# Performance work log

Measured on AMD Instinct MI355X. Metric: run time of the kernel, lower is better.

## Reference

```python
import jax, jax.numpy as jnp
import numpy as np

HARD_ANGLE = 15.0  # degrees, from PMLoss __init__ default
NUM_CLASSES = 22
NUM_POINTS = 2048
BATCH = 32


def quat_to_rotmat(q):
    # q: [..., 4] in (w, x, y, z) order (PoseCNN convention); assumes unit norm
    w, x, y, z = q[..., 0], q[..., 1], q[..., 2], q[..., 3]
    R = jnp.stack([
        1 - 2 * (y * y + z * z), 2 * (x * y - z * w), 2 * (x * z + y * w),
        2 * (x * y + z * w), 1 - 2 * (x * x + z * z), 2 * (y * z - x * w),
        2 * (x * z - y * w), 2 * (y * z + x * w), 1 - 2 * (x * x + y * y)],
        axis=-1)
    return R.reshape(q.shape[:-1] + (3, 3))


def smooth_l1(x):
    ax = jnp.abs(x)
    return jnp.where(ax < 1.0, 0.5 * x * x, ax - 0.5)


def setup_inputs() -> dict:
    key = jax.random.key(0)
    k1, k2, k3, k4 = jax.random.split(key, 4)
    B, C, P = BATCH, NUM_CLASSES, NUM_POINTS
    # unit quaternions per (sample, class)
    q_pred = jax.random.normal(k1, (B, C, 4), dtype=jnp.float32)
    q_pred = q_pred / jnp.linalg.norm(q_pred, axis=-1, keepdims=True)
    q_gt = jax.random.normal(k2, (B, C, 4), dtype=jnp.float32)
    q_gt = q_gt / jnp.linalg.norm(q_gt, axis=-1, keepdims=True)
    prediction = q_pred.reshape(B, 4 * C)
    target = q_gt.reshape(B, 4 * C)
    # one active class per sample: weight block of ones at that class
    cls = jax.random.randint(k3, (B,), 1, C)  # skip background class 0
    weight = jnp.zeros((B, C, 4), dtype=jnp.float32)
    weight = weight.at[jnp.arange(B), cls, :].set(1.0).reshape(B, 4 * C)
    # model point clouds, roughly object-scale (~10 cm)
    points = 0.1 * jax.random.normal(k4, (C, P, 3), dtype=jnp.float32)
    # half the classes symmetric
    symmetry = (jnp.arange(C) % 2).astype(jnp.float32)
    return {"prediction": prediction, "target": target, "weight": weight,
            "points": points, "symmetry": symmetry}


def reference(prediction, target, weight, points, symmetry):
    B = prediction.shape[0]
    C = symmetry.shape[0]
    P = points.shape[1]
    # class per sample = first class with weight > 0 (CUDA scans stride-4 w slot)
    wsel = weight.reshape(B, C, 4)[:, :, 0]           # [B, C]
    cls = jnp.argmax(wsel > 0, axis=1)                # [B]
    valid = (jnp.max(wsel, axis=1) > 0)               # [B] samples with a class
    bidx = jnp.arange(B)
    q_pred = prediction.reshape(B, C, 4)[bidx, cls]   # [B, 4]
    q_gt = target.reshape(B, C, 4)[bidx, cls]         # [B, 4]
    R_pred = quat_to_rotmat(q_pred)                   # [B, 3, 3]
    R_gt = quat_to_rotmat(q_gt)
    pts = points[cls]                                 # [B, P, 3]
    p_pred = jnp.einsum('bij,bpj->bpi', R_pred, pts)  # [B, P, 3]
    p_gt = jnp.einsum('bij,bpj->bpi', R_gt, pts)      # [B, P, 3]
    # angular distance between quaternions, in degrees
    dot = jnp.abs(jnp.sum(q_pred * q_gt, axis=1))
    ang = 2.0 * jnp.arccos(jnp.clip(dot, 0.0, 1.0)) * (180.0 / jnp.pi)
    use_closest = (symmetry[cls] > 0) & (ang > HARD_ANGLE)  # [B]
    # pairwise squared distances without materializing [B,P,P,3]
    d2 = (jnp.sum(p_pred * p_pred, axis=-1)[:, :, None]
          + jnp.sum(p_gt * p_gt, axis=-1)[:, None, :]
          - 2.0 * jnp.einsum('bpi,bqi->bpq', p_pred, p_gt))  # [B, P, P]
    nn_idx = jnp.argmin(d2, axis=-1)                         # [B, P]
    p_gt_nn = jnp.take_along_axis(p_gt, nn_idx[..., None], axis=1)
    matched = jnp.where(use_closest[:, None, None], p_gt_nn, p_gt)
    diff = p_pred - matched                                   # [B, P, 3]
    per_sample = jnp.sum(smooth_l1(diff), axis=(1, 2)) * valid.astype(diff.dtype)
    loss = jnp.sum(per_sample) / jnp.asarray(B * P, dtype=diff.dtype)
    return loss
```

## Files before the change

### kernel.cpp

```cpp
#include <hip/hip_runtime.h>

#define NPTS 2048
#define QC 32
#define G  (NPTS / QC)
#define RP 8
#define HARD_COS 0.9914448613738104f
#define META_FLOATS 8
#define PRED_OFF 1024


__global__ __launch_bounds__(256) void pm_setup(const float* __restrict__ pred,
                                                const float* __restrict__ tgt,
                                                const float* __restrict__ wgt,
                                                const float* __restrict__ sym,
                                                const float* __restrict__ points,
                                                float* __restrict__ ws,
                                                float* __restrict__ out,
                                                int B, int C, int gt_off) {
    const int b = blockIdx.y;
    const int side = blockIdx.x;

    int cls = 0; float valid = 0.0f;
    for (int c = 0; c < C; ++c) {
        if (wgt[b * 4 * C + c * 4] > 0.0f) { cls = c; valid = 1.0f; break; }
    }

    const float* q = (side == 0 ? pred : tgt) + b * 4 * C + cls * 4;
    const float w = q[0], x = q[1], y = q[2], z = q[3];
    const float m0 = 1.f - 2.f * (y * y + z * z);
    const float m1 = 2.f * (x * y - z * w);
    const float m2 = 2.f * (x * z + y * w);
    const float m3 = 2.f * (x * y + z * w);
    const float m4 = 1.f - 2.f * (x * x + z * z);
    const float m5 = 2.f * (y * z - x * w);
    const float m6 = 2.f * (x * z - y * w);
    const float m7 = 2.f * (y * z + x * w);
    const float m8 = 1.f - 2.f * (x * x + y * y);

    const float* pts = points + (size_t)cls * NPTS * 3;
    float4* dst = (float4*)(ws + (side == 0 ? PRED_OFF : gt_off)) + (size_t)b * NPTS;
    const int tid = threadIdx.x;
    if (valid != 0.0f) {
#pragma unroll
        for (int r = 0; r < RP; ++r) {
            int i = r * 256 + tid;
            float px = pts[i * 3 + 0], py = pts[i * 3 + 1], pz = pts[i * 3 + 2];
            float ax = m0 * px + m1 * py + m2 * pz;
            float ay = m3 * px + m4 * py + m5 * pz;
            float az = m6 * px + m7 * py + m8 * pz;
            float ww = (side == 0) ? 0.0f : (ax * ax + ay * ay + az * az);
            dst[i] = make_float4(ax, ay, az, ww);
        }
    }

    if (side == 0 && tid == 0) {
        const float* qp = pred + b * 4 * C + cls * 4;
        const float* qg = tgt  + b * 4 * C + cls * 4;
        float dot = fabsf(qp[0] * qg[0] + qp[1] * qg[1] + qp[2] * qg[2] + qp[3] * qg[3]);
        dot = fminf(fmaxf(dot, 0.0f), 1.0f);
        float uc = (sym[cls] > 0.0f && dot < HARD_COS) ? 1.0f : 0.0f;
        ws[b * META_FLOATS + 0] = valid;
        ws[b * META_FLOATS + 1] = uc;
        if (b == 0) out[0] = 0.0f;
    }
}

__global__ __launch_bounds__(256) void pm_partial(float* __restrict__ ws,
                                                  int gt_off, int cand_off) {
    const int b  = blockIdx.y;
    const int qc = blockIdx.x;
    if (ws[b * META_FLOATS + 0] == 0.0f || ws[b * META_FLOATS + 1] == 0.0f) return;

    const float4* pred_rot = (const float4*)(ws + PRED_OFF) + (size_t)b * NPTS;
    const float4* gt_rot   = (const float4*)(ws + gt_off)   + (size_t)b * NPTS;
    const int tid = threadIdx.x;

    __shared__ float4 gt[G];
    if (tid < G) gt[tid] = gt_rot[qc * G + tid];
    __syncthreads();

    float nx[RP], ny[RP], nz[RP], bd[RP];
    int bi[RP];
#pragma unroll
    for (int r = 0; r < RP; ++r) {
        float4 pp = pred_rot[r * 256 + tid];
        nx[r] = -2.0f * pp.x; ny[r] = -2.0f * pp.y; nz[r] = -2.0f * pp.z;
        bd[r] = 3.4e38f; bi[r] = 0;
    }

#pragma unroll 4
    for (int j = 0; j < G; ++j) {
        float4 g = gt[j];
#pragma unroll
        for (int r = 0; r < RP; ++r) {
            float d = __fmaf_rn(nx[r], g.x,
                      __fmaf_rn(ny[r], g.y,
                      __fmaf_rn(nz[r], g.z, g.w)));
            if (d < bd[r]) { bd[r] = d; bi[r] = j; }
        }
    }

    float2* cand = (float2*)(ws + cand_off) + ((size_t)b * QC + qc) * NPTS;
#pragma unroll
    for (int r = 0; r < RP; ++r) {
        int p = r * 256 + tid;
        cand[p] = make_float2(bd[r], (float)(qc * G + bi[r]));
    }
}

__device__ __forceinline__ float smooth_l1(float x) {
    float ax = fabsf(x);
    return (ax < 1.0f) ? 0.5f * x * x : ax - 0.5f;
}

__global__ __launch_bounds__(256) void pm_final(float* __restrict__ ws,
                                                float* __restrict__ out,
                                                int gt_off, int cand_off,
                                                float inv_bp) {
    __shared__ float partial[4];
    const int b = blockIdx.y;
    const int tid = threadIdx.x;
    float acc = 0.0f;

    if (ws[b * META_FLOATS + 0] != 0.0f) {
        const float4* pred_rot = (const float4*)(ws + PRED_OFF) + (size_t)b * NPTS;
        const float4* gt_rot   = (const float4*)(ws + gt_off)   + (size_t)b * NPTS;
        const int p = blockIdx.x * 256 + tid;
        float4 pp = pred_rot[p];
        float4 g;
        if (ws[b * META_FLOATS + 1] != 0.0f) {
            const float2* cand = (const float2*)(ws + cand_off) + (size_t)b * QC * NPTS + p;
            float bd = 3.4e38f; int bq = 0;
#pragma unroll
            for (int qc = 0; qc < QC; ++qc) {
                float2 cq = cand[(size_t)qc * NPTS];
                if (cq.x < bd) { bd = cq.x; bq = (int)cq.y; }
            }
            g = gt_rot[bq];
        } else {
            g = gt_rot[p];
        }
        acc = smooth_l1(pp.x - g.x) + smooth_l1(pp.y - g.y) + smooth_l1(pp.z - g.z);
    }

    for (int off = 32; off > 0; off >>= 1) acc += __shfl_down(acc, off);
    if ((tid & 63) == 0) partial[tid >> 6] = acc;
    __syncthreads();
    if (tid == 0) {
        float s = partial[0] + partial[1] + partial[2] + partial[3];
        atomicAdd(out, s * inv_bp);
    }
}

extern "C" void kernel_launch(void* const* d_in, const int* in_sizes, int n_in,
                              void* d_out, int out_size, void* d_ws, size_t ws_size,
                              hipStream_t stream) {
    const float* pred = (const float*)d_in[0];
    const float* tgt  = (const float*)d_in[1];
    const float* wgt  = (const float*)d_in[2];
    const float* pts  = (const float*)d_in[3];
    const float* sym  = (const float*)d_in[4];
    float* out = (float*)d_out;
    float* ws  = (float*)d_ws;

    const int C = in_sizes[4];
    const int B = in_sizes[0] / (4 * C);

    const int gt_off   = PRED_OFF + B * NPTS * 4;
    const int cand_off = gt_off   + B * NPTS * 4;

    dim3 gridS(2, B);
    pm_setup<<<gridS, 256, 0, stream>>>(pred, tgt, wgt, sym, pts, ws, out, B, C, gt_off);
    dim3 gridP(QC, B);
    pm_partial<<<gridP, 256, 0, stream>>>(ws, gt_off, cand_off);
    dim3 gridF(NPTS / 256, B);
    pm_final<<<gridF, 256, 0, stream>>>(ws, out, gt_off, cand_off,
                                        1.0f / (float)(B * NPTS));
}
```

Baseline: 107.1 us.

## Fuse setup kernel into scan and final by recomputing rotated points on the fly

Removes the separate setup kernel that wrote rotated pred/gt point clouds to workspace. The scan and final kernels now derive the class and use-closest flag themselves, build the rotation matrices, and rotate points directly from the model point cloud. This saves one kernel launch and the workspace round-trip, at the cost of redundant meta scans and rotations in every block.

Result: faster. 104.8 us (-2.1%).

```diff
diff --git a/kernel.cpp b/kernel.cpp
--- a/kernel.cpp
+++ b/kernel.cpp
@@ -5,88 +5,89 @@
 #define G  (NPTS / QC)
 #define RP 8
 #define HARD_COS 0.9914448613738104f
-#define META_FLOATS 8
-#define PRED_OFF 1024
 
 
-__global__ __launch_bounds__(256) void pm_setup(const float* __restrict__ pred,
-                                                const float* __restrict__ tgt,
-                                                const float* __restrict__ wgt,
-                                                const float* __restrict__ sym,
-                                                const float* __restrict__ points,
-                                                float* __restrict__ ws,
-                                                float* __restrict__ out,
-                                                int B, int C, int gt_off) {
-    const int b = blockIdx.y;
-    const int side = blockIdx.x;
+struct Meta { int cls; bool valid; bool uc; };
 
-    int cls = 0; float valid = 0.0f;
+__device__ __forceinline__ Meta get_meta(const float* __restrict__ pred,
+                                         const float* __restrict__ tgt,
+                                         const float* __restrict__ wgt,
+                                         const float* __restrict__ sym,
+                                         int b, int C) {
+    Meta m; m.cls = 0; m.valid = false;
     for (int c = 0; c < C; ++c) {
-        if (wgt[b * 4 * C + c * 4] > 0.0f) { cls = c; valid = 1.0f; break; }
+        if (wgt[b * 4 * C + c * 4] > 0.0f) { m.cls = c; m.valid = true; break; }
     }
-
-    const float* q = (side == 0 ? pred : tgt) + b * 4 * C + cls * 4;
-    const float w = q[0], x = q[1], y = q[2], z = q[3];
-    const float m0 = 1.f - 2.f * (y * y + z * z);
-    const float m1 = 2.f * (x * y - z * w);
-    const float m2 = 2.f * (x * z + y * w);
-    const float m3 = 2.f * (x * y + z * w);
-    const float m4 = 1.f - 2.f * (x * x + z * z);
-    const float m5 = 2.f * (y * z - x * w);
-    const float m6 = 2.f * (x * z - y * w);
-    const float m7 = 2.f * (y * z + x * w);
-    const float m8 = 1.f - 2.f * (x * x + y * y);
-
-    const float* pts = points + (size_t)cls * NPTS * 3;
-    float4* dst = (float4*)(ws + (side == 0 ? PRED_OFF : gt_off)) + (size_t)b * NPTS;
-    const int tid = threadIdx.x;
-    if (valid != 0.0f) {
-#pragma unroll
-        for (int r = 0; r < RP; ++r) {
-            int i = r * 256 + tid;
-            float px = pts[i * 3 + 0], py = pts[i * 3 + 1], pz = pts[i * 3 + 2];
-            float ax = m0 * px + m1 * py + m2 * pz;
-            float ay = m3 * px + m4 * py + m5 * pz;
-            float az = m6 * px + m7 * py + m8 * pz;
-            float ww = (side == 0) ? 0.0f : (ax * ax + ay * ay + az * az);
-            dst[i] = make_float4(ax, ay, az, ww);
-        }
-    }
-
-    if (side == 0 && tid == 0) {
-        const float* qp = pred + b * 4 * C + cls * 4;
-        const float* qg = tgt  + b * 4 * C + cls * 4;
-        float dot = fabsf(qp[0] * qg[0] + qp[1] * qg[1] + qp[2] * qg[2] + qp[3] * qg[3]);
-        dot = fminf(fmaxf(dot, 0.0f), 1.0f);
-        float uc = (sym[cls] > 0.0f && dot < HARD_COS) ? 1.0f : 0.0f;
-        ws[b * META_FLOATS + 0] = valid;
-        ws[b * META_FLOATS + 1] = uc;
-        if (b == 0) out[0] = 0.0f;
-    }
+    const float* qp = pred + b * 4 * C + m.cls * 4;
+    const float* qg = tgt  + b * 4 * C + m.cls * 4;
+    float dot = fabsf(qp[0] * qg[0] + qp[1] * qg[1] + qp[2] * qg[2] + qp[3] * qg[3]);
+    dot = fminf(fmaxf(dot, 0.0f), 1.0f);
+    m.uc = m.valid && (sym[m.cls] > 0.0f) && (dot < HARD_COS);
+    return m;
 }
 
-__global__ __launch_bounds__(256) void pm_partial(float* __restrict__ ws,
-                                                  int gt_off, int cand_off) {
+__device__ __forceinline__ void quat_rotmat(const float* __restrict__ q, float* m) {
+    float w = q[0], x = q[1], y = q[2], z = q[3];
+    m[0] = 1.f - 2.f * (y * y + z * z);
+    m[1] = 2.f * (x * y - z * w);
+    m[2] = 2.f * (x * z + y * w);
+    m[3] = 2.f * (x * y + z * w);
+    m[4] = 1.f - 2.f * (x * x + z * z);
+    m[5] = 2.f * (y * z - x * w);
+    m[6] = 2.f * (x * z - y * w);
+    m[7] = 2.f * (y * z + x * w);
+    m[8] = 1.f - 2.f * (x * x + y * y);
+}
+
+__device__ __forceinline__ float smooth_l1(float x) {
+    float ax = fabsf(x);
+    return (ax < 1.0f) ? 0.5f * x * x : ax - 0.5f;
+}
+
+__global__ __launch_bounds__(256) void pm_scan(const float* __restrict__ pred,
+                                               const float* __restrict__ tgt,
+                                               const float* __restrict__ wgt,
+                                               const float* __restrict__ sym,
+                                               const float* __restrict__ points,
+                                               float* __restrict__ ws,
+                                               float* __restrict__ out, int C) {
     const int b  = blockIdx.y;
     const int qc = blockIdx.x;
-    if (ws[b * META_FLOATS + 0] == 0.0f || ws[b * META_FLOATS + 1] == 0.0f) return;
-
-    const float4* pred_rot = (const float4*)(ws + PRED_OFF) + (size_t)b * NPTS;
-    const float4* gt_rot   = (const float4*)(ws + gt_off)   + (size_t)b * NPTS;
     const int tid = threadIdx.x;
 
+    if (b == 0 && qc == 0 && tid == 0) out[0] = 0.0f;
+
+    Meta mt = get_meta(pred, tgt, wgt, sym, b, C);
+    if (!mt.valid || !mt.uc) return;
+
+    float Rp[9], Rg[9];
+    quat_rotmat(pred + b * 4 * C + mt.cls * 4, Rp);
+    quat_rotmat(tgt  + b * 4 * C + mt.cls * 4, Rg);
+    const float* pts = points + (size_t)mt.cls * NPTS * 3;
+
     __shared__ float4 gt[G];
-    if (tid < G) gt[tid] = gt_rot[qc * G + tid];
-    __syncthreads();
+    if (tid < G) {
+        int i = qc * G + tid;
+        float x = pts[i * 3 + 0], y = pts[i * 3 + 1], z = pts[i * 3 + 2];
+        float ax = Rg[0] * x + Rg[1] * y + Rg[2] * z;
+        float ay = Rg[3] * x + Rg[4] * y + Rg[5] * z;
+        float az = Rg[6] * x + Rg[7] * y + Rg[8] * z;
+        gt[tid] = make_float4(ax, ay, az, ax * ax + ay * ay + az * az);
+    }
 
     float nx[RP], ny[RP], nz[RP], bd[RP];
     int bi[RP];
 #pragma unroll
     for (int r = 0; r < RP; ++r) {
-        float4 pp = pred_rot[r * 256 + tid];
-        nx[r] = -2.0f * pp.x; ny[r] = -2.0f * pp.y; nz[r] = -2.0f * pp.z;
+        int p = r * 256 + tid;
+        float x = pts[p * 3 + 0], y = pts[p * 3 + 1], z = pts[p * 3 + 2];
+        float ppx = Rp[0] * x + Rp[1] * y + Rp[2] * z;
+        float ppy = Rp[3] * x + Rp[4] * y + Rp[5] * z;
+        float ppz = Rp[6] * x + Rp[7] * y + Rp[8] * z;
+        nx[r] = -2.0f * ppx; ny[r] = -2.0f * ppy; nz[r] = -2.0f * ppz;
         bd[r] = 3.4e38f; bi[r] = 0;
     }
+    __syncthreads();
 
 #pragma unroll 4
     for (int j = 0; j < G; ++j) {
@@ -100,7 +101,7 @@
         }
     }
 
-    float2* cand = (float2*)(ws + cand_off) + ((size_t)b * QC + qc) * NPTS;
+    float2* cand = (float2*)ws + ((size_t)b * QC + qc) * NPTS;
 #pragma unroll
     for (int r = 0; r < RP; ++r) {
         int p = r * 256 + tid;
@@ -108,39 +109,47 @@
     }
 }
 
-__device__ __forceinline__ float smooth_l1(float x) {
-    float ax = fabsf(x);
-    return (ax < 1.0f) ? 0.5f * x * x : ax - 0.5f;
-}
-
-__global__ __launch_bounds__(256) void pm_final(float* __restrict__ ws,
+__global__ __launch_bounds__(256) void pm_final(const float* __restrict__ pred,
+                                                const float* __restrict__ tgt,
+                                                const float* __restrict__ wgt,
+                                                const float* __restrict__ sym,
+                                                const float* __restrict__ points,
+                                                const float* __restrict__ ws,
                                                 float* __restrict__ out,
-                                                int gt_off, int cand_off,
-                                                float inv_bp) {
+                                                int C, float inv_bp) {
     __shared__ float partial[4];
     const int b = blockIdx.y;
     const int tid = threadIdx.x;
     float acc = 0.0f;
 
-    if (ws[b * META_FLOATS + 0] != 0.0f) {
-        const float4* pred_rot = (const float4*)(ws + PRED_OFF) + (size_t)b * NPTS;
-        const float4* gt_rot   = (const float4*)(ws + gt_off)   + (size_t)b * NPTS;
+    Meta mt = get_meta(pred, tgt, wgt, sym, b, C);
+    if (mt.valid) {
+        float Rp[9], Rg[9];
+        quat_rotmat(pred + b * 4 * C + mt.cls * 4, Rp);
+        quat_rotmat(tgt  + b * 4 * C + mt.cls * 4, Rg);
+        const float* pts = points + (size_t)mt.cls * NPTS * 3;
         const int p = blockIdx.x * 256 + tid;
-        float4 pp = pred_rot[p];
-        float4 g;
-        if (ws[b * META_FLOATS + 1] != 0.0f) {
-            const float2* cand = (const float2*)(ws + cand_off) + (size_t)b * QC * NPTS + p;
-            float bd = 3.4e38f; int bq = 0;
+
+        float x = pts[p * 3 + 0], y = pts[p * 3 + 1], z = pts[p * 3 + 2];
+        float ppx = Rp[0] * x + Rp[1] * y + Rp[2] * z;
+        float ppy = Rp[3] * x + Rp[4] * y + Rp[5] * z;
+        float ppz = Rp[6] * x + Rp[7] * y + Rp[8] * z;
+
+        int q = p;
+        if (mt.uc) {
+            const float2* cand = (const float2*)ws + (size_t)b * QC * NPTS + p;
+            float bd = 3.4e38f; q = 0;
 #pragma unroll
-            for (int qc = 0; qc < QC; ++qc) {
-                float2 cq = cand[(size_t)qc * NPTS];
-                if (cq.x < bd) { bd = cq.x; bq = (int)cq.y; }
+            for (int c = 0; c < QC; ++c) {
+                float2 cq = cand[(size_t)c * NPTS];
+                if (cq.x < bd) { bd = cq.x; q = (int)cq.y; }
             }
-            g = gt_rot[bq];
-        } else {
-            g = gt_rot[p];
         }
-        acc = smooth_l1(pp.x - g.x) + smooth_l1(pp.y - g.y) + smooth_l1(pp.z - g.z);
+        float qx = pts[q * 3 + 0], qy = pts[q * 3 + 1], qz = pts[q * 3 + 2];
+        float gx = Rg[0] * qx + Rg[1] * qy + Rg[2] * qz;
+        float gy = Rg[3] * qx + Rg[4] * qy + Rg[5] * qz;
+        float gz = Rg[6] * qx + Rg[7] * qy + Rg[8] * qz;
+        acc = smooth_l1(ppx - gx) + smooth_l1(ppy - gy) + smooth_l1(ppz - gz);
     }
 
     for (int off = 32; off > 0; off >>= 1) acc += __shfl_down(acc, off);
@@ -166,14 +175,9 @@
     const int C = in_sizes[4];
     const int B = in_sizes[0] / (4 * C);
 
-    const int gt_off   = PRED_OFF + B * NPTS * 4;
-    const int cand_off = gt_off   + B * NPTS * 4;
-
-    dim3 gridS(2, B);
-    pm_setup<<<gridS, 256, 0, stream>>>(pred, tgt, wgt, sym, pts, ws, out, B, C, gt_off);
-    dim3 gridP(QC, B);
-    pm_partial<<<gridP, 256, 0, stream>>>(ws, gt_off, cand_off);
+    dim3 gridS(QC, B);
+    pm_scan<<<gridS, 256, 0, stream>>>(pred, tgt, wgt, sym, pts, ws, out, C);
     dim3 gridF(NPTS / 256, B);
-    pm_final<<<gridF, 256, 0, stream>>>(ws, out, gt_off, cand_off,
-                                        1.0f / (float)(B * NPTS));
+    pm_final<<<gridF, 256, 0, stream>>>(pred, tgt, wgt, sym, pts, ws, out,
+                                        C, 1.0f / (float)(B * NPTS));
 }
```
